# Optimization experiments

Hardware: AMD Instinct MI355X
Metric: run time of the kernel (lower is better)

## Reference

```python
import jax, jax.numpy as jnp
import numpy as np

H, L, N1, N2, N3 = 256, 141, 9, 34, 98
B, S = 64, 512

def setup_inputs() -> dict:
    key = jax.random.key(0)
    cnt = [0]
    def nrm(shape, s=0.05):
        cnt[0] += 1
        return jax.random.normal(jax.random.fold_in(key, cnt[0]), shape, jnp.float32) * s
    d = {}
    d['inputs'] = jax.random.randint(jax.random.fold_in(key, 1000), (B, S), 0, 30522)
    d['text_hidden'] = nrm((B, S, 768), 1.0)
    d['label_encoding'] = nrm((L, H), 1.0)
    d['w12'] = (jax.random.uniform(jax.random.fold_in(key, 1001), (N1, N2)) < 0.3).astype(jnp.float32)
    d['w23'] = (jax.random.uniform(jax.random.fold_in(key, 1002), (N2, N3)) < 0.3).astype(jnp.float32)
    d['fre12'] = jax.random.uniform(jax.random.fold_in(key, 1003), (N1, N2), jnp.float32)
    d['fre23'] = jax.random.uniform(jax.random.fold_in(key, 1004), (N2, N3), jnp.float32)
    for name in ['wi1', 'wf1', 'wo1', 'wu1', 'wi2', 'wf2', 'wo2', 'wu2']:
        d[name + '_W'] = nrm((H, H)); d[name + '_b'] = nrm((H,))
    for name in ['ui1', 'uf1', 'uo1', 'uu1', 'ui2', 'uf2', 'uo2', 'uu2']:
        d[name + '_W'] = nrm((H, H))
    d['mix_W'] = nrm((3 * H, H)); d['mix_b'] = nrm((H,))
    d['tt_W'] = nrm((768, H)); d['tt_b'] = nrm((H,))
    d['A'] = nrm((L, L)); d['Wp'] = nrm((H, H))
    d['out_W'] = nrm((L * H, L)); d['out_b'] = nrm((L,))
    return d

def reference(inputs, text_hidden, label_encoding, w12, w23, fre12, fre23,
              wi1_W, wi1_b, wf1_W, wf1_b, wo1_W, wo1_b, wu1_W, wu1_b,
              wi2_W, wi2_b, wf2_W, wf2_b, wo2_W, wo2_b, wu2_W, wu2_b,
              ui1_W, uf1_W, uo1_W, uu1_W, ui2_W, uf2_W, uo2_W, uu2_W,
              mix_W, mix_b, tt_W, tt_b, A, Wp, out_W, out_b):
    sig, tanh = jax.nn.sigmoid, jnp.tanh
    v1 = label_encoding[:N1]          # [N1,H]
    v2 = label_encoding[N1:N1 + N2]   # [N2,H]
    v3 = label_encoding[N1 + N2:]     # [N3,H]
    w21, w32 = w12.T, w23.T
    # --- top-down tree-LSTM (suffix 1) ---
    i11 = sig(v1 @ wi1_W + wi1_b); o11 = sig(v1 @ wo1_W + wo1_b); u11 = tanh(v1 @ wu1_W + wu1_b)
    c11 = i11 * u11; h11 = o11 * tanh(c11)
    h21t = w21 @ h11
    i21 = sig(v2 @ wi1_W + wi1_b + h21t @ ui1_W)
    f21 = sig(v2 @ wf1_W + wf1_b + h21t @ uf1_W)
    o21 = sig(v2 @ wo1_W + wo1_b + h21t @ uo1_W)
    u21 = tanh(v2 @ wu1_W + wu1_b + h21t @ uu1_W)
    c21 = i21 * u21 + f21 * (w21 @ c11); h21 = o21 * tanh(c21)
    h31t = w32 @ h21
    i31 = sig(v3 @ wi1_W + wi1_b + h31t @ ui1_W)
    f31 = sig(v3 @ wf1_W + wf1_b + h31t @ uf1_W)
    o31 = sig(v3 @ wo1_W + wo1_b + h31t @ uo1_W)
    u31 = tanh(v3 @ wu1_W + wu1_b + h31t @ uu1_W)
    c31 = i31 * u31 + f31 * (w32 @ c21); h31 = o31 * tanh(c31)
    # --- bottom-up tree-LSTM (suffix 2) ---
    i32 = sig(v3 @ wi2_W + wi2_b); o32 = sig(v3 @ wo2_W + wo2_b); u32 = tanh(v3 @ wu2_W + wu2_b)
    c32 = i32 * u32; h32 = o32 * tanh(c32)
    h22t = fre23 @ h32
    i22 = sig(v2 @ wi2_W + wi2_b + h22t @ ui2_W)
    f22 = sig((w32 @ v2) @ wf2_W + wf2_b + h32 @ uf2_W)   # [N3,H]
    o22 = sig(v2 @ wo2_W + wo2_b + h22t @ uo2_W)
    u22 = tanh(v2 @ wu2_W + wu2_b + h22t @ uu2_W)
    c22 = i22 * u22 + w23 @ (f22 * c32); h22 = o22 * tanh(c22)
    h12t = fre12 @ h22
    i12 = sig(v1 @ wi2_W + wi2_b + h12t @ ui2_W)
    f12 = sig((w21 @ v1) @ wf2_W + wf2_b + h22 @ uf2_W)   # [N2,H]
    o12 = sig(v1 @ wo2_W + wo2_b + h12t @ uo2_W)
    u12 = tanh(v1 @ wu2_W + wu2_b + h12t @ uu2_W)
    c12 = i12 * u12 + w12 @ (f12 * c22); h12 = o12 * tanh(c12)
    h1 = jnp.concatenate([h11, h12], axis=1)
    h2 = jnp.concatenate([h21, h22], axis=1)
    h3 = jnp.concatenate([h31, h32], axis=1)
    le = jnp.concatenate([h1, h2, h3], axis=0)            # [L,2H]
    temp = jax.nn.relu(A @ label_encoding @ Wp)           # [L,H]
    le = jnp.concatenate([le, temp], axis=1) @ mix_W + mix_b  # [L,H]
    # --- masked cross-attention pooling over text ---
    text = tanh(text_hidden @ tt_W + tt_b)                # [B,S,H]
    att = jnp.einsum('lh,bsh->bls', le, text)             # [B,L,S]
    pad = jnp.where((inputs == 0) | (inputs == 101) | (inputs == 102), -jnp.inf, 0.0).astype(text.dtype)
    att = jax.nn.softmax(att + pad[:, None, :], axis=2)
    features = jnp.einsum('bls,bsh->blh', att, text).reshape(inputs.shape[0], -1)  # [B,L*H]
    return sig(features @ out_W + out_b)                  # [B,L]
```

## Files before the change

kernel.cpp:

```cpp
#include <hip/hip_runtime.h>
#include <math.h>

static constexpr int H = 256, L = 141, N1 = 9, N2 = 34, N3 = 98;
static constexpr int B = 64, S = 512;

typedef __attribute__((ext_vector_type(8))) _Float16 f16x8;
typedef __attribute__((ext_vector_type(4))) float f32x4;

__device__ inline unsigned short f2h(float x) {
    _Float16 h = (_Float16)x;
    return __builtin_bit_cast(unsigned short, h);
}
__device__ inline float sigf(float x) { return 1.f / (1.f + __expf(-x)); }

__device__ inline void gload_lds16(const void* g, void* l) {
    __builtin_amdgcn_global_load_lds(
        (const __attribute__((address_space(1))) void*)g,
        (__attribute__((address_space(3))) void*)l, 16, 0, 0);
}

__global__ __launch_bounds__(256) void prep(
    const float* __restrict__ ttW, unsigned short* __restrict__ Bt,
    const float* __restrict__ outW, unsigned short* __restrict__ outWh)
{
    __shared__ unsigned short Tl[32][257];
    __shared__ unsigned short T2[64 * 65];
    const int tid = threadIdx.x;
    if (blockIdx.x < 24) {
        const int t = blockIdx.x;
        #pragma unroll
        for (int p = 0; p < 32; p++) {
            int lin = p * 256 + tid;
            int r = lin >> 8, c = lin & 255;
            Tl[r][c] = f2h(ttW[(long)(t * 32 + r) * 256 + c]);
        }
        __syncthreads();
        unsigned short v[32];
        #pragma unroll
        for (int kin = 0; kin < 32; kin++) v[kin] = Tl[kin][tid];
        uint4* dst = (uint4*)(Bt + ((long)t * 256 + tid) * 32);
        #pragma unroll
        for (int q = 0; q < 4; q++) dst[q] = ((const uint4*)v)[q];
    } else {
        const int u = blockIdx.x - 24;
        const int r0 = (u % 564) * 64, c0 = (u / 564) * 64;
        const int R = 36096, C = 141;
        #pragma unroll
        for (int p = 0; p < 16; p++) {
            int lin = p * 256 + tid;
            int r = lin >> 6, c = lin & 63;
            int gc = c0 + c;
            float v = (gc < C) ? outW[(long)(r0 + r) * C + gc] : 0.f;
            T2[c * 65 + r] = f2h(v);
        }
        __syncthreads();
        #pragma unroll
        for (int p = 0; p < 16; p++) {
            int lin = p * 256 + tid;
            int c = lin >> 6, r = lin & 63;
            if (c0 + c < C)
                outWh[(long)(c0 + c) * R + r0 + r] = T2[c * 65 + r];
        }
    }
}

__global__ __launch_bounds__(512, 4) void text_gemm3(
    const float* __restrict__ Af,
    const unsigned short* __restrict__ Bt,
    const float* __restrict__ bias,
    unsigned short* __restrict__ outH,
    unsigned short* __restrict__ outHT)
{
    __shared__ unsigned short smem[28672];
    unsigned short* As = smem;
    unsigned short* Bs = smem + 4096;
    unsigned short* T  = smem;

    const int tid  = threadIdx.x;
    const int wave = tid >> 6, lane = tid & 63;
    const int quad = lane >> 4, l16 = lane & 15;
    const int m0 = blockIdx.x * 64;
    const int wm = (wave >> 2) * 32;
    const int wn = (wave & 3) * 64;

    const int arow = tid >> 3;
    const int ac16 = tid & 7;
    const float* aSrc = Af + (long)(m0 + arow) * 768 + ac16 * 4;
    const int ac8d = ac16 ^ ((arow & 3) << 1);
    const int aWoff = arow * 32 + ac8d * 4;

    const int bsc = (lane & 3) ^ ((lane >> 3) & 3);
    const long bSrcOff0 = (long)(wave * 32 + (lane >> 2)) * 32 + bsc * 8;
    const long bSrcOff1 = bSrcOff0 + 16 * 32;
    const int bDst0 = (wave * 32) * 32, bDst1 = (wave * 32 + 16) * 32;

    int aro[2], bro[4];
    #pragma unroll
    for (int i = 0; i < 2; i++) {
        int r = wm + i * 16 + l16;
        aro[i] = r * 32 + ((quad * 2) ^ ((r & 3) << 1)) * 4;
    }
    #pragma unroll
    for (int j = 0; j < 4; j++) {
        int n = wn + j * 16 + l16;
        bro[j] = n * 32 + ((quad ^ ((n >> 1) & 3)) << 3);
    }

    f32x4 acc[2][4] = {};
    float4 ar0, ar1;

    auto issueB = [&](int kt, int pb) {
        const unsigned short* src = Bt + (long)kt * 8192;
        unsigned short* d = Bs + pb * 8192;
        gload_lds16(src + bSrcOff0, d + bDst0);
        gload_lds16(src + bSrcOff1, d + bDst1);
    };
    auto writeA = [&](const float4& v, int pa) {
        unsigned int p0 = f2h(v.x) | ((unsigned int)f2h(v.y) << 16);
        unsigned int p1 = f2h(v.z) | ((unsigned int)f2h(v.w) << 16);
        *(uint2*)&As[pa * 2048 + aWoff] = make_uint2(p0, p1);
    };

    ar0 = *(const float4*)(aSrc + 0 * 32);
    issueB(0, 0);
    ar1 = *(const float4*)(aSrc + 1 * 32);
    issueB(1, 1);
    asm volatile("s_waitcnt vmcnt(5)" ::: "memory");
    writeA(ar0, 0);
    asm volatile("s_waitcnt vmcnt(3)" ::: "memory");
    asm volatile("s_waitcnt lgkmcnt(0)" ::: "memory");
    asm volatile("s_barrier" ::: "memory");

    auto body = [&](int t, float4& arIn, float4& arOut, int pa, int pr) {
        int kt2 = (t + 2 <= 23) ? t + 2 : 23;
        arOut = *(const float4*)(aSrc + kt2 * 32);
        f16x8 a[2], b[4];
        const unsigned short* ab = As + pa * 2048;
        const unsigned short* bb = Bs + pr * 8192;
        #pragma unroll
        for (int i = 0; i < 2; i++) a[i] = *(const f16x8*)&ab[aro[i]];
        #pragma unroll
        for (int j = 0; j < 4; j++) b[j] = *(const f16x8*)&bb[bro[j]];
        #pragma unroll
        for (int i = 0; i < 2; i++)
            #pragma unroll
            for (int j = 0; j < 4; j++)
                acc[i][j] = __builtin_amdgcn_mfma_f32_16x16x32_f16(
                    a[i], b[j], acc[i][j], 0, 0, 0);
        asm volatile("s_waitcnt vmcnt(3)" ::: "memory");
        writeA(arIn, pa ^ 1);
        int pw = pr + 2; if (pw >= 3) pw -= 3;
        issueB(kt2, pw);
        asm volatile("s_waitcnt vmcnt(3)" ::: "memory");
        asm volatile("s_waitcnt lgkmcnt(0)" ::: "memory");
        asm volatile("s_barrier" ::: "memory");
    };

    int pr = 0;
    #pragma unroll 1
    for (int t = 0; t < 24; t += 2) {
        body(t,     ar1, ar0, t & 1 ? 1 : 0, pr);
        int pr1 = pr + 1; if (pr1 >= 3) pr1 -= 3;
        body(t + 1, ar0, ar1, 1, pr1);
        pr = pr1 + 1; if (pr >= 3) pr -= 3;
    }
    asm volatile("s_waitcnt vmcnt(0)" ::: "memory");
    __syncthreads();

    float bv[4];
    #pragma unroll
    for (int j = 0; j < 4; j++) bv[j] = bias[wn + j * 16 + l16];

    #pragma unroll
    for (int i = 0; i < 2; i++) {
        #pragma unroll
        for (int j = 0; j < 4; j++) {
            const int mlb = wm + i * 16 + quad * 4;
            const int n   = wn + j * 16 + l16;
            unsigned short hv[4];
            #pragma unroll
            for (int r = 0; r < 4; r++) {
                float v = tanhf(acc[i][j][r] + bv[j]);
                hv[r] = f2h(v);
                outH[(long)(m0 + mlb + r) * 256 + n] = hv[r];
            }
            uint2 p;
            p.x = hv[0] | ((unsigned int)hv[1] << 16);
            p.y = hv[2] | ((unsigned int)hv[3] << 16);
            *(uint2*)&T[n * 72 + mlb] = p;
        }
    }
    __syncthreads();
    {
        const int bb2 = m0 >> 9, s0 = m0 & 511;
        const int n = tid >> 1, half = tid & 1;
        const uint4* src = (const uint4*)&T[n * 72 + half * 32];
        uint4* dst = (uint4*)&outHT[((long)bb2 * 256 + n) * 512 + s0 + half * 32];
        dst[0] = src[0]; dst[1] = src[1];
        dst[2] = src[2]; dst[3] = src[3];
    }
}

__global__ __launch_bounds__(256) void gates_pre(
    const float* __restrict__ le,
    const float* W0, const float* W1, const float* W2, const float* W3,
    const float* W4, const float* W5, const float* W6,
    const float* b0, const float* b1, const float* b2, const float* b3,
    const float* b4, const float* b5, const float* b6,
    const float* __restrict__ Amat, const float* __restrict__ w23,
    const float* __restrict__ w12, const float* __restrict__ Wp,
    const float* __restrict__ wf2_W,
    float* __restrict__ G, float* __restrict__ tmpP,
    float* __restrict__ wv2f, float* __restrict__ wv1f)
{
    __shared__ float smem[768];
    const int tid = threadIdx.x;
    const int nl = tid & 63, ks = tid >> 6;
    if (blockIdx.x < 28 * 141) {
        const int u = blockIdx.x;
        const int bx = u % 28, m = u / 28;
        const int j = bx >> 2, x = bx & 3, n = x * 64 + nl;
        float* ls = smem; float* red = smem + 256;
        ls[tid] = le[(long)m * 256 + tid];
        __syncthreads();
        const float *W, *bb;
        switch (j) {
            case 0: W = W0; bb = b0; break;  case 1: W = W1; bb = b1; break;
            case 2: W = W2; bb = b2; break;  case 3: W = W3; bb = b3; break;
            case 4: W = W4; bb = b4; break;  case 5: W = W5; bb = b5; break;
            default: W = W6; bb = b6;
        }
        float a0 = 0, a1 = 0, a2 = 0, a3 = 0;
        for (int k = ks; k + 12 < 256; k += 16) {
            long o = (long)k * 256 + n;
            a0 += ls[k] * W[o];        a1 += ls[k + 4] * W[o + 1024];
            a2 += ls[k + 8] * W[o + 2048]; a3 += ls[k + 12] * W[o + 3072];
        }
        red[tid] = a0 + a1 + a2 + a3;
        __syncthreads();
        if (ks == 0)
            G[((long)j * 141 + m) * 256 + n] =
                red[nl] + red[64 + nl] + red[128 + nl] + red[192 + nl] + bb[n];
    } else {
        const int u = blockIdx.x - 28 * 141;
        const int x = u % 4, y = u / 4, n = x * 64 + nl;
        int job, m, K1;
        if (y < 141)      { job = 0; m = y;       K1 = 141; }
        else if (y < 239) { job = 1; m = y - 141; K1 = 34; }
        else              { job = 2; m = y - 239; K1 = 9; }
        float* cs = smem; float* t = smem + 256; float* red = smem + 512;
        if (tid < K1)
            cs[tid] = (job == 0) ? Amat[(long)m * 141 + tid]
                    : (job == 1) ? w23[(long)tid * 98 + m]
                                 : w12[(long)tid * 34 + m];
        __syncthreads();
        const float* s1 = (job == 1) ? le + 9 * 256 : le;
        float acc = 0;
        #pragma unroll 4
        for (int k = 0; k < K1; k++) acc += cs[k] * s1[(long)k * 256 + tid];
        t[tid] = acc;
        __syncthreads();
        const float* W = (job == 0) ? Wp : wf2_W;
        float a0 = 0, a1 = 0, a2 = 0, a3 = 0;
        for (int k = ks; k + 12 < 256; k += 16) {
            long o = (long)k * 256 + n;
            a0 += t[k] * W[o];        a1 += t[k + 4] * W[o + 1024];
            a2 += t[k + 8] * W[o + 2048]; a3 += t[k + 12] * W[o + 3072];
        }
        red[tid] = a0 + a1 + a2 + a3;
        __syncthreads();
        if (ks == 0) {
            float tot = red[nl] + red[64 + nl] + red[128 + nl] + red[192 + nl];
            if (job == 0)      tmpP[(long)m * 256 + n] = fmaxf(tot, 0.f);
            else if (job == 1) wv2f[(long)m * 256 + n] = tot;
            else               wv1f[(long)m * 256 + n] = tot;
        }
    }
}

__global__ __launch_bounds__(256) void ew1(
    const float* __restrict__ G, float* __restrict__ h11, float* __restrict__ c11,
    float* __restrict__ h32, float* __restrict__ c32)
{
    int y = blockIdx.x, n = threadIdx.x;
    if (y < 9) {
        int m = y;
        float iv = sigf(G[(0L * 141 + m) * 256 + n]);
        float ov = sigf(G[(2L * 141 + m) * 256 + n]);
        float uv = tanhf(G[(3L * 141 + m) * 256 + n]);
        float cv = iv * uv;
        c11[m * 256 + n] = cv; h11[m * 256 + n] = ov * tanhf(cv);
    } else {
        int r = y - 9, grow = 43 + r;
        float iv = sigf(G[(4L * 141 + grow) * 256 + n]);
        float ov = sigf(G[(5L * 141 + grow) * 256 + n]);
        float uv = tanhf(G[(6L * 141 + grow) * 256 + n]);
        float cv = iv * uv;
        c32[r * 256 + n] = cv; h32[r * 256 + n] = ov * tanhf(cv);
    }
}

__global__ __launch_bounds__(256) void chain_mm(int phase,
    const float* __restrict__ w12, const float* __restrict__ w23,
    const float* __restrict__ fre23, const float* __restrict__ fre12,
    const float* __restrict__ h11, const float* __restrict__ c11,
    const float* __restrict__ h32,
    const float* __restrict__ h21, const float* __restrict__ c21,
    const float* __restrict__ h22,
    const float* __restrict__ wv2f, const float* __restrict__ wv1f,
// ... 153 lines not shown
    const float* __restrict__ tmpP, const float* __restrict__ mix_W,
    const float* __restrict__ mix_b, unsigned short* __restrict__ le_h)
{
    __shared__ float ls[768];
    __shared__ float red[256];
    const int x = blockIdx.x, l = blockIdx.y;
    const int tid = threadIdx.x, nl = tid & 63, ks = tid >> 6, n = x * 64 + nl;
    const float *pa, *pb; int r;
    if (l < 9)       { pa = h11; pb = h12; r = l; }
    else if (l < 43) { pa = h21; pb = h22; r = l - 9; }
    else             { pa = h31; pb = h32; r = l - 43; }
    for (int j = tid; j < 768; j += 256) {
        float v;
        if (j < 256)      v = pa[r * 256 + j];
        else if (j < 512) v = pb[r * 256 + (j - 256)];
        else              v = tmpP[l * 256 + (j - 512)];
        ls[j] = v;
    }
    __syncthreads();
    float a0 = 0, a1 = 0, a2 = 0, a3 = 0;
    for (int k = ks; k + 12 < 768; k += 16) {
        long o = (long)k * 256 + n;
        a0 += ls[k] * mix_W[o];        a1 += ls[k + 4] * mix_W[o + 1024];
        a2 += ls[k + 8] * mix_W[o + 2048]; a3 += ls[k + 12] * mix_W[o + 3072];
    }
    red[tid] = a0 + a1 + a2 + a3;
    __syncthreads();
    if (ks == 0) {
        float tot = red[nl] + red[64 + nl] + red[128 + nl] + red[192 + nl] + mix_b[n];
        le_h[(long)l * 256 + n] = f2h(tot);
    }
}

__global__ __launch_bounds__(512, 1) void att_logits2(
    const unsigned short* __restrict__ le_h,
    const unsigned short* __restrict__ text_h,
    const int* __restrict__ tokens,
    unsigned short* __restrict__ att_h)
{
    __shared__ unsigned short A_s[64 * 256];
    __shared__ unsigned short Bs[2][512 * 32];
    __shared__ float redm[8][32];
    __shared__ float reds[8][32];
    const int tid  = threadIdx.x;
    const int wave = tid >> 6, lane = tid & 63;
    const int quad = lane >> 4, l16 = lane & 15;
    const int m0 = blockIdx.x * 64;
    const int b  = blockIdx.y;
    const int wm = (wave >> 2) * 32;
    const int wn = (wave & 3) * 128;

    const int bsc = (lane & 3) ^ ((lane >> 3) & 3);
    const long bOffBase = (long)(b * 512 + wave * 64 + (lane >> 2)) * 256 + bsc * 8;
    const int bDstBase = (wave * 64) * 32;
    auto issueB = [&](int kt, int pb) {
        #pragma unroll
        for (int q = 0; q < 4; q++)
            gload_lds16(text_h + bOffBase + (long)q * 16 * 256 + kt * 32,
                        &Bs[pb][bDstBase + q * 16 * 32]);
    };

    int abase[2], axm[2], bro[8];
    #pragma unroll
    for (int i = 0; i < 2; i++) {
        int r = wm + i * 16 + l16;
        abase[i] = r * 256; axm[i] = r & 7;
    }
    #pragma unroll
    for (int j = 0; j < 8; j++) {
        int n = wn + j * 16 + l16;
        bro[j] = n * 32 + ((quad ^ ((n >> 1) & 3)) << 3);
    }

    #pragma unroll
    for (int p = 0; p < 4; p++) {
        int row = p * 16 + (tid >> 5);
        int c   = tid & 31;
        int grow = m0 + row; if (grow > L - 1) grow = L - 1;
        gload_lds16(le_h + (long)grow * 256 + ((c ^ (row & 7)) << 3),
                    A_s + p * 4096 + wave * 512);
    }
    issueB(0, 0);
    issueB(1, 1);
    asm volatile("s_waitcnt vmcnt(4)" ::: "memory");
    asm volatile("s_barrier" ::: "memory");

    f32x4 acc[2][8] = {};
    #pragma unroll 1
    for (int t = 0; t < 8; t++) {
        const int pb = t & 1;
        f16x8 a[2], bf[8];
        #pragma unroll
        for (int i = 0; i < 2; i++)
            a[i] = *(const f16x8*)&A_s[abase[i] + (((t * 4 + quad) ^ axm[i]) << 3)];
        const unsigned short* bb = &Bs[pb][0];
        #pragma unroll
        for (int j = 0; j < 8; j++) bf[j] = *(const f16x8*)&bb[bro[j]];
        #pragma unroll
        for (int i = 0; i < 2; i++)
            #pragma unroll
            for (int j = 0; j < 8; j++)
                acc[i][j] = __builtin_amdgcn_mfma_f32_16x16x32_f16(
                    a[i], bf[j], acc[i][j], 0, 0, 0);
        if (t < 7) {
            asm volatile("s_waitcnt lgkmcnt(0)" ::: "memory");
            asm volatile("s_barrier" ::: "memory");
            int kt2 = (t + 2 <= 7) ? t + 2 : 7;
            issueB(kt2, pb);
            asm volatile("s_waitcnt vmcnt(4)" ::: "memory");
            asm volatile("s_barrier" ::: "memory");
        }
    }
    asm volatile("s_waitcnt vmcnt(0)" ::: "memory");

    float mvv[8];
    #pragma unroll
    for (int j = 0; j < 8; j++) {
        int gs = wn + j * 16 + l16;
        int tok = tokens[(long)b * 512 + gs];
        mvv[j] = (tok == 0 || tok == 101 || tok == 102) ? 1e30f : 0.f;
    }
    #pragma unroll
    for (int i = 0; i < 2; i++)
        #pragma unroll
        for (int j = 0; j < 8; j++)
            #pragma unroll
            for (int r = 0; r < 4; r++) acc[i][j][r] -= mvv[j];

// ... 27 lines not shown
    for (int i = 0; i < 2; i++)
        #pragma unroll
        for (int j = 0; j < 8; j++)
            #pragma unroll
            for (int r = 0; r < 4; r++) {
                float e = __expf(acc[i][j][r] - M[i][r]);
                acc[i][j][r] = e;
                psum[i][r] += e;
            }
    #pragma unroll
    for (int i = 0; i < 2; i++)
        #pragma unroll
        for (int r = 0; r < 4; r++) {
            float v = psum[i][r];
            #pragma unroll
            for (int d = 1; d <= 8; d <<= 1) v += __shfl_xor(v, d);
            if (l16 == 0) reds[wave][i * 16 + quad * 4 + r] = v;
        }
    __syncthreads();
    #pragma unroll
    for (int i = 0; i < 2; i++)
        #pragma unroll
        for (int r = 0; r < 4; r++) {
            int rl = i * 16 + quad * 4 + r;
            float s = reds[wgrp][rl] + reds[wgrp + 1][rl]
                    + reds[wgrp + 2][rl] + reds[wgrp + 3][rl];
            M[i][r] = 1.f / s;
        }

    #pragma unroll
    for (int i = 0; i < 2; i++)
        #pragma unroll
        for (int r = 0; r < 4; r++) {
            int gm = m0 + wm + i * 16 + quad * 4 + r;
            if (gm < L) {
                unsigned short* orow = att_h + ((long)b * L + gm) * 512;
                #pragma unroll
                for (int j = 0; j < 8; j++)
                    orow[wn + j * 16 + l16] = f2h(acc[i][j][r] * M[i][r]);
            }
        }
}

__global__ __launch_bounds__(512, 4) void att_pv(
    const unsigned short* __restrict__ att_h,
    const unsigned short* __restrict__ text_hT,
    unsigned short* __restrict__ feat_h)
{
    __shared__ unsigned short As[2 * 64 * 64];
    __shared__ unsigned short Bs[3][256 * 32];
    const int tid  = threadIdx.x;
    const int wave = tid >> 6, lane = tid & 63;
    const int quad = lane >> 4, l16 = lane & 15;
    const int m0 = blockIdx.x * 64;
    const int b  = blockIdx.y;
    const int wm = (wave >> 2) * 32;
    const int wn = (wave & 3) * 64;

    int arow = m0 + wave * 8 + (lane >> 3); if (arow > L - 1) arow = L - 1;
    const int asc = (lane & 7) ^ (lane >> 3);
    const unsigned short* aSrc = att_h + ((long)b * L + arow) * 512 + asc * 8;
    const int aDst = wave * 512;
    auto issueA = [&](int ka, int pa) {
        gload_lds16(aSrc + ka * 64, &As[pa * 4096 + aDst]);
    };

    const int bsc = (lane & 3) ^ ((lane >> 3) & 3);
    const long bOff0 = ((long)b * 256 + wave * 32 + (lane >> 2)) * 512 + bsc * 8;
    const long bOff1 = bOff0 + 16 * 512;
    const int bDst0 = (wave * 32) * 32, bDst1 = bDst0 + 16 * 32;
    auto issueB = [&](int kt, int pb) {
        gload_lds16(text_hT + bOff0 + kt * 32, &Bs[pb][bDst0]);
        gload_lds16(text_hT + bOff1 + kt * 32, &Bs[pb][bDst1]);
    };

    int aro[2], axm[2], bro[4];
    #pragma unroll
    for (int i = 0; i < 2; i++) {
        int r = wm + i * 16 + l16;
        aro[i] = r * 64; axm[i] = r & 7;
    }
    #pragma unroll
    for (int j = 0; j < 4; j++) {
        int n = wn + j * 16 + l16;
        bro[j] = n * 32 + ((quad ^ ((n >> 1) & 3)) << 3);
    }

    issueA(0, 0);
    issueB(0, 0);
    issueB(1, 1);
    asm volatile("s_waitcnt vmcnt(2)" ::: "memory");
    asm volatile("s_barrier" ::: "memory");

    f32x4 acc[2][4] = {};
    #pragma unroll 1
    for (int t = 0; t < 16; t++) {
        const int pa = (t >> 1) & 1, pr = t % 3, sub = t & 1;
        f16x8 a[2], bfr[4];
        const unsigned short* ab = &As[pa * 4096];
        #pragma unroll
        for (int i = 0; i < 2; i++)
            a[i] = *(const f16x8*)&ab[aro[i] + (((sub * 4 + quad) ^ axm[i]) << 3)];
        const unsigned short* bb = &Bs[pr][0];
        #pragma unroll
        for (int j = 0; j < 4; j++) bfr[j] = *(const f16x8*)&bb[bro[j]];
        #pragma unroll
        for (int i = 0; i < 2; i++)
            #pragma unroll
            for (int j = 0; j < 4; j++)
                acc[i][j] = __builtin_amdgcn_mfma_f32_16x16x32_f16(
                    a[i], bfr[j], acc[i][j], 0, 0, 0);
        if (t < 15) {
            if (sub == 0) {
                int ka = (t >> 1) + 1; if (ka > 7) ka = 7;
                issueA(ka, pa ^ 1);
            }
            int kb = t + 2; if (kb > 15) kb = 15;
            issueB(kb, (t + 2) % 3);
            if (sub == 0) {
                asm volatile("s_waitcnt vmcnt(3)" ::: "memory");
            } else {
                asm volatile("s_waitcnt vmcnt(2)" ::: "memory");
            }
            asm volatile("s_barrier" ::: "memory");
        }
    }
    asm volatile("s_waitcnt vmcnt(0)" ::: "memory");

    #pragma unroll
    for (int i = 0; i < 2; i++)
        #pragma unroll
        for (int j = 0; j < 4; j++)
            #pragma unroll
            for (int r = 0; r < 4; r++) {
                int gm = m0 + wm + i * 16 + quad * 4 + r;
                if (gm < L) {
                    int h = wn + j * 16 + l16;
                    feat_h[(long)b * (L * H) + (long)gm * 256 + h] =
                        f2h(acc[i][j][r]);
                }
            }
}

template<int EPI, bool CONVA, int IM>
__global__ __launch_bounds__(256) void gemm_mfma(
    const void* __restrict__ Aptr, int lda, long strA,
    const unsigned short* __restrict__ Bp, int ldb, long strB,
    float* __restrict__ C, int ldc, long strC,
    int M, int N, int K,
    const float* __restrict__ bias,
    const int* __restrict__ tokens,
    unsigned short* __restrict__ outH,
    unsigned short* __restrict__ outHT,
    int kChunk)
{
    __shared__ unsigned short A_s[32 * IM * 32];
    __shared__ unsigned short B_s[128 * 32];
    const int tid  = threadIdx.x;
    const int wave = tid >> 6, lane = tid & 63;
    const int quad = lane >> 4, l16 = lane & 15;
    const int bz = blockIdx.z;
    const int m0 = blockIdx.y * (32 * IM), n0 = blockIdx.x * 128;
    const int wm = (wave & 1) * (16 * IM), wn = (wave >> 1) * 64;

    long aBase, bBase;
    int kBeg, kEnd;
    if (EPI == 4) { aBase = 0; bBase = 0; kBeg = bz * kChunk; kEnd = kBeg + kChunk; }
    else { aBase = (long)bz * strA; bBase = (long)bz * strB; kBeg = 0; kEnd = K; }

    f32x4 acc[IM][4] = {};

    for (int k0 = kBeg; k0 < kEnd; k0 += 32) {
// ... 104 lines not shown
    const float* uo1_W = (const float*)d_in[25], *uu1_W = (const float*)d_in[26];
    const float* ui2_W = (const float*)d_in[27], *uf2_W = (const float*)d_in[28];
    const float* uo2_W = (const float*)d_in[29], *uu2_W = (const float*)d_in[30];
    const float* mix_W = (const float*)d_in[31], *mix_b = (const float*)d_in[32];
    const float* tt_W  = (const float*)d_in[33], *tt_b  = (const float*)d_in[34];
    const float* Amat  = (const float*)d_in[35], *Wp    = (const float*)d_in[36];
    const float* out_W = (const float*)d_in[37], *out_b = (const float*)d_in[38];
    float* out = (float*)d_out;

    float* ws = (float*)d_ws;
    float* att     = ws; ws += (long)B * L * S;
    unsigned short* text_h  = (unsigned short*)ws; ws += (long)B * S * H / 2;
    unsigned short* text_hT = (unsigned short*)ws; ws += (long)B * S * H / 2;
    unsigned short* att_h   = (unsigned short*)ws; ws += (long)B * L * S / 2;
    unsigned short* tt_Wt   = (unsigned short*)ws; ws += 768 * H / 2;
    unsigned short* le_h    = (unsigned short*)ws; ws += L * H / 2 + 4;
    unsigned short* out_Wh  = (unsigned short*)ws; ws += (long)L * 36096 / 2;
    unsigned short* feat_h  = (unsigned short*)ws; ws += (long)B * L * H / 2;
    float* outacc = ws; ws += (long)B * L * 141;
    float* G    = ws; ws += 7 * 141 * 256;
    float* tmpP = ws; ws += L * H;
    float* wv2f = ws; ws += N3 * H;
    float* wv1f = ws; ws += N2 * H;
    float* h11  = ws; ws += N1 * H;  float* c11  = ws; ws += N1 * H;
    float* h21  = ws; ws += N2 * H;  float* c21  = ws; ws += N2 * H;
    float* h21t = ws; ws += N2 * H;  float* c21p = ws; ws += N2 * H;
    float* h31  = ws; ws += N3 * H;  float* h31t = ws; ws += N3 * H;
    float* c31p = ws; ws += N3 * H;
    float* h32  = ws; ws += N3 * H;  float* c32  = ws; ws += N3 * H;
    float* h22  = ws; ws += N2 * H;  float* c22  = ws; ws += N2 * H;
    float* h22t = ws; ws += N2 * H;  float* fcb  = ws; ws += N3 * H;
    float* h12  = ws; ws += N1 * H;  float* h12t = ws; ws += N1 * H;
    float* fc2b = ws; ws += N2 * H;
    (void)att;

    prep<<<24 + 564 * 3, 256, 0, stream>>>(tt_W, tt_Wt, out_W, out_Wh);
    text_gemm3<<<512, 512, 0, stream>>>(
        text_hidden, tt_Wt, tt_b, text_h, text_hT);
    gates_pre<<<28 * 141 + 4 * 273, 256, 0, stream>>>(label_enc,
        wi1_W, wf1_W, wo1_W, wu1_W, wi2_W, wo2_W, wu2_W,
        wi1_b, wf1_b, wo1_b, wu1_b, wi2_b, wo2_b, wu2_b,
        Amat, w23, w12, Wp, wf2_W, G, tmpP, wv2f, wv1f);
    ew1<<<107, 256, 0, stream>>>(G, h11, c11, h32, c32);
    chain_mm<<<dim3(4, 200), 256, 0, stream>>>(0, w12, w23, fre23, fre12,
        h11, c11, h32, h21, c21, h22, wv2f, wv1f, wf2_b, uf2_W, c32, c22,
        h21t, c21p, h22t, fcb, h31t, c31p, h12t, fc2b);
    lstm_fused<<<dim3(4, 68), 256, 0, stream>>>(0, G,
        h21t, c21p, h22t, fcb, h31t, c31p, h12t, fc2b, w23, w12,
        ui1_W, uf1_W, uo1_W, uu1_W, ui2_W, uo2_W, uu2_W,
        h21, c21, h22, c22, h31, h12);
    chain_mm<<<dim3(4, 239), 256, 0, stream>>>(1, w12, w23, fre23, fre12,
        h11, c11, h32, h21, c21, h22, wv2f, wv1f, wf2_b, uf2_W, c32, c22,
        h21t, c21p, h22t, fcb, h31t, c31p, h12t, fc2b);
    lstm_fused<<<dim3(4, 107), 256, 0, stream>>>(1, G,
        h21t, c21p, h22t, fcb, h31t, c31p, h12t, fc2b, w23, w12,
        ui1_W, uf1_W, uo1_W, uu1_W, ui2_W, uo2_W, uu2_W,
        h21, c21, h22, c22, h31, h12);
    mix_mm<<<dim3(4, 141), 256, 0, stream>>>(h11, h12, h21, h22, h31, h32,
        tmpP, mix_W, mix_b, le_h);
    att_logits2<<<dim3(3, 64), 512, 0, stream>>>(
        le_h, text_h, inputs, att_h);
    att_pv<<<dim3(3, 64), 512, 0, stream>>>(att_h, text_hT, feat_h);
    gemm_mfma<4, false, 2><<<dim3(2, 1, 141), 256, 0, stream>>>(
        feat_h, L * H, 0, out_Wh, L * H, 0, outacc, L, (long)B * L,
        B, L, L * H, nullptr, nullptr, nullptr, nullptr, 256);
    out_final<<<(B * L + 255) / 256, 256, 0, stream>>>(outacc, out_b, out, B * L, 141);
}
```

Baseline: 439.3 us.

## Enlarge text GEMM tile to 128 rows with 1024-thread blocks

The text projection GEMM now uses 1024-thread blocks covering 128 rows each, so the B-operand tile loaded into LDS is shared by twice as many rows and each thread issues one B load per stage instead of two. Wait counts, A buffer sizes and the transposed-output epilogue are reworked, with the epilogue run in two halves through the shared staging buffer. The trade-off is only 256 blocks at one block per CU, which reduces occupancy and adds barriers in the epilogue.

New measurement: 443.1 us. About the same (+0.8%).

```diff
diff --git a/kernel.cpp b/kernel.cpp
--- a/kernel.cpp
+++ b/kernel.cpp
@@ -64,22 +64,22 @@
     }
 }
 
-__global__ __launch_bounds__(512, 4) void text_gemm3(
+__global__ __launch_bounds__(1024, 1) void text_gemm4(
     const float* __restrict__ Af,
     const unsigned short* __restrict__ Bt,
     const float* __restrict__ bias,
     unsigned short* __restrict__ outH,
     unsigned short* __restrict__ outHT)
 {
-    __shared__ unsigned short smem[28672];
+    __shared__ unsigned short smem[32768];
     unsigned short* As = smem;
-    unsigned short* Bs = smem + 4096;
+    unsigned short* Bs = smem + 8192;
     unsigned short* T  = smem;
 
     const int tid  = threadIdx.x;
     const int wave = tid >> 6, lane = tid & 63;
     const int quad = lane >> 4, l16 = lane & 15;
-    const int m0 = blockIdx.x * 64;
+    const int m0 = blockIdx.x * 128;
     const int wm = (wave >> 2) * 32;
     const int wn = (wave & 3) * 64;
 
@@ -90,9 +90,8 @@
     const int aWoff = arow * 32 + ac8d * 4;
 
     const int bsc = (lane & 3) ^ ((lane >> 3) & 3);
-    const long bSrcOff0 = (long)(wave * 32 + (lane >> 2)) * 32 + bsc * 8;
-    const long bSrcOff1 = bSrcOff0 + 16 * 32;
-    const int bDst0 = (wave * 32) * 32, bDst1 = (wave * 32 + 16) * 32;
+    const long bSrcOff = (long)(wave * 16 + (lane >> 2)) * 32 + bsc * 8;
+    const int bDst = (wave * 16) * 32;
 
     int aro[2], bro[4];
     #pragma unroll
@@ -110,24 +109,21 @@
     float4 ar0, ar1;
 
     auto issueB = [&](int kt, int pb) {
-        const unsigned short* src = Bt + (long)kt * 8192;
-        unsigned short* d = Bs + pb * 8192;
-        gload_lds16(src + bSrcOff0, d + bDst0);
-        gload_lds16(src + bSrcOff1, d + bDst1);
+        gload_lds16(Bt + (long)kt * 8192 + bSrcOff, Bs + pb * 8192 + bDst);
     };
     auto writeA = [&](const float4& v, int pa) {
         unsigned int p0 = f2h(v.x) | ((unsigned int)f2h(v.y) << 16);
         unsigned int p1 = f2h(v.z) | ((unsigned int)f2h(v.w) << 16);
-        *(uint2*)&As[pa * 2048 + aWoff] = make_uint2(p0, p1);
+        *(uint2*)&As[pa * 4096 + aWoff] = make_uint2(p0, p1);
     };
 
     ar0 = *(const float4*)(aSrc + 0 * 32);
     issueB(0, 0);
     ar1 = *(const float4*)(aSrc + 1 * 32);
     issueB(1, 1);
-    asm volatile("s_waitcnt vmcnt(5)" ::: "memory");
+    asm volatile("s_waitcnt vmcnt(3)" ::: "memory");
     writeA(ar0, 0);
-    asm volatile("s_waitcnt vmcnt(3)" ::: "memory");
+    asm volatile("s_waitcnt vmcnt(2)" ::: "memory");
     asm volatile("s_waitcnt lgkmcnt(0)" ::: "memory");
     asm volatile("s_barrier" ::: "memory");
 
@@ -135,7 +131,7 @@
         int kt2 = (t + 2 <= 23) ? t + 2 : 23;
         arOut = *(const float4*)(aSrc + kt2 * 32);
         f16x8 a[2], b[4];
-        const unsigned short* ab = As + pa * 2048;
+        const unsigned short* ab = As + pa * 4096;
         const unsigned short* bb = Bs + pr * 8192;
         #pragma unroll
         for (int i = 0; i < 2; i++) a[i] = *(const f16x8*)&ab[aro[i]];
@@ -147,11 +143,11 @@
             for (int j = 0; j < 4; j++)
                 acc[i][j] = __builtin_amdgcn_mfma_f32_16x16x32_f16(
                     a[i], b[j], acc[i][j], 0, 0, 0);
-        asm volatile("s_waitcnt vmcnt(3)" ::: "memory");
+        asm volatile("s_waitcnt vmcnt(2)" ::: "memory");
         writeA(arIn, pa ^ 1);
         int pw = pr + 2; if (pw >= 3) pw -= 3;
         issueB(kt2, pw);
-        asm volatile("s_waitcnt vmcnt(3)" ::: "memory");
+        asm volatile("s_waitcnt vmcnt(2)" ::: "memory");
         asm volatile("s_waitcnt lgkmcnt(0)" ::: "memory");
         asm volatile("s_barrier" ::: "memory");
     };
@@ -159,7 +155,7 @@
     int pr = 0;
     #pragma unroll 1
     for (int t = 0; t < 24; t += 2) {
-        body(t,     ar1, ar0, t & 1 ? 1 : 0, pr);
+        body(t,     ar1, ar0, 0, pr);
         int pr1 = pr + 1; if (pr1 >= 3) pr1 -= 3;
         body(t + 1, ar0, ar1, 1, pr1);
         pr = pr1 + 1; if (pr >= 3) pr -= 3;
@@ -170,34 +166,41 @@
     float bv[4];
     #pragma unroll
     for (int j = 0; j < 4; j++) bv[j] = bias[wn + j * 16 + l16];
-
-    #pragma unroll
-    for (int i = 0; i < 2; i++) {
-        #pragma unroll
-        for (int j = 0; j < 4; j++) {
-            const int mlb = wm + i * 16 + quad * 4;
-            const int n   = wn + j * 16 + l16;
-            unsigned short hv[4];
-            #pragma unroll
-            for (int r = 0; r < 4; r++) {
-                float v = tanhf(acc[i][j][r] + bv[j]);
-                hv[r] = f2h(v);
-                outH[(long)(m0 + mlb + r) * 256 + n] = hv[r];
+    const int bb2 = m0 >> 9, s0base = m0 & 511;
+    const int myhalf = wave >> 3;
+
+    #pragma unroll
+    for (int h = 0; h < 2; h++) {
+        __syncthreads();
+        if (myhalf == h) {
+            #pragma unroll
+            for (int i = 0; i < 2; i++) {
+                #pragma unroll
+                for (int j = 0; j < 4; j++) {
+                    const int mlb = wm + i * 16 + quad * 4;
+                    const int n   = wn + j * 16 + l16;
+                    unsigned short hv[4];
+                    #pragma unroll
+                    for (int r = 0; r < 4; r++) {
+                        float v = tanhf(acc[i][j][r] + bv[j]);
+                        hv[r] = f2h(v);
+                        outH[(long)(m0 + mlb + r) * 256 + n] = hv[r];
+                    }
+                    uint2 p;
+                    p.x = hv[0] | ((unsigned int)hv[1] << 16);
+                    p.y = hv[2] | ((unsigned int)hv[3] << 16);
+                    *(uint2*)&T[n * 72 + (mlb - h * 64)] = p;
+                }
             }
-            uint2 p;
-            p.x = hv[0] | ((unsigned int)hv[1] << 16);
-            p.y = hv[2] | ((unsigned int)hv[3] << 16);
-            *(uint2*)&T[n * 72 + mlb] = p;
-        }
-    }
-    __syncthreads();
-    {
-        const int bb2 = m0 >> 9, s0 = m0 & 511;
-        const int n = tid >> 1, half = tid & 1;
-        const uint4* src = (const uint4*)&T[n * 72 + half * 32];
-        uint4* dst = (uint4*)&outHT[((long)bb2 * 256 + n) * 512 + s0 + half * 32];
-        dst[0] = src[0]; dst[1] = src[1];
-        dst[2] = src[2]; dst[3] = src[3];
+        }
+        __syncthreads();
+        {
+            const int n = tid >> 2, q = tid & 3;
+            const uint4* src = (const uint4*)&T[n * 72 + q * 16];
+            uint4* dst = (uint4*)&outHT[((long)bb2 * 256 + n) * 512
+                                        + s0base + h * 64 + q * 16];
+            dst[0] = src[0]; dst[1] = src[1];
+        }
     }
 }
 
@@ -928,7 +931,7 @@
     (void)att;
 
     prep<<<24 + 564 * 3, 256, 0, stream>>>(tt_W, tt_Wt, out_W, out_Wh);
-    text_gemm3<<<512, 512, 0, stream>>>(
+    text_gemm4<<<256, 1024, 0, stream>>>(
         text_hidden, tt_Wt, tt_b, text_h, text_hT);
     gates_pre<<<28 * 141 + 4 * 273, 256, 0, stream>>>(label_enc,
         wi1_W, wf1_W, wo1_W, wu1_W, wi2_W, wo2_W, wu2_W,
```

## Fuse attention logits with PV matmul and merge prep with gate precompute

Applied to the files above, without the earlier changes.

Merges the attention-logit/softmax kernel with the P·V kernel so normalized probabilities stay in LDS (swizzled) instead of round-tripping through global memory. Also merges the weight-conversion prep kernel with the gate pre-activation kernel into one launch. A body() argument in text_gemm3 is simplified to a constant 0. This removes launches and the att_h global traffic, at the cost of larger LDS use in the fused attention kernel, which has launch bounds of 512 threads with min 1 block.

New measurement: 426.5 us. 1.03x faster.

```diff
diff --git a/kernel.cpp b/kernel.cpp
--- a/kernel.cpp
+++ b/kernel.cpp
@@ -19,30 +19,42 @@
         (__attribute__((address_space(3))) void*)l, 16, 0, 0);
 }
 
-__global__ __launch_bounds__(256) void prep(
+__global__ __launch_bounds__(256) void prep_gates(
     const float* __restrict__ ttW, unsigned short* __restrict__ Bt,
-    const float* __restrict__ outW, unsigned short* __restrict__ outWh)
+    const float* __restrict__ outW, unsigned short* __restrict__ outWh,
+    const float* __restrict__ le,
+    const float* W0, const float* W1, const float* W2, const float* W3,
+    const float* W4, const float* W5, const float* W6,
+    const float* b0, const float* b1, const float* b2, const float* b3,
+    const float* b4, const float* b5, const float* b6,
+    const float* __restrict__ Amat, const float* __restrict__ w23,
+    const float* __restrict__ w12, const float* __restrict__ Wp,
+    const float* __restrict__ wf2_W,
+    float* __restrict__ G, float* __restrict__ tmpP,
+    float* __restrict__ wv2f, float* __restrict__ wv1f)
 {
-    __shared__ unsigned short Tl[32][257];
-    __shared__ unsigned short T2[64 * 65];
+    __shared__ float sf[4112];
+    unsigned short* su = (unsigned short*)sf;
     const int tid = threadIdx.x;
-    if (blockIdx.x < 24) {
-        const int t = blockIdx.x;
+    const int bx = blockIdx.x;
+    const int nl = tid & 63, ks = tid >> 6;
+    if (bx < 24) {
+        const int t = bx;
         #pragma unroll
         for (int p = 0; p < 32; p++) {
             int lin = p * 256 + tid;
             int r = lin >> 8, c = lin & 255;
-            Tl[r][c] = f2h(ttW[(long)(t * 32 + r) * 256 + c]);
+            su[r * 257 + c] = f2h(ttW[(long)(t * 32 + r) * 256 + c]);
         }
         __syncthreads();
         unsigned short v[32];
         #pragma unroll
-        for (int kin = 0; kin < 32; kin++) v[kin] = Tl[kin][tid];
+        for (int kin = 0; kin < 32; kin++) v[kin] = su[kin * 257 + tid];
         uint4* dst = (uint4*)(Bt + ((long)t * 256 + tid) * 32);
         #pragma unroll
         for (int q = 0; q < 4; q++) dst[q] = ((const uint4*)v)[q];
-    } else {
-        const int u = blockIdx.x - 24;
+    } else if (bx < 24 + 1692) {
+        const int u = bx - 24;
         const int r0 = (u % 564) * 64, c0 = (u / 564) * 64;
         const int R = 36096, C = 141;
         #pragma unroll
@@ -51,7 +63,7 @@
             int r = lin >> 6, c = lin & 63;
             int gc = c0 + c;
             float v = (gc < C) ? outW[(long)(r0 + r) * C + gc] : 0.f;
-            T2[c * 65 + r] = f2h(v);
+            su[c * 65 + r] = f2h(v);
         }
         __syncthreads();
         #pragma unroll
@@ -59,7 +71,66 @@
             int lin = p * 256 + tid;
             int c = lin >> 6, r = lin & 63;
             if (c0 + c < C)
-                outWh[(long)(c0 + c) * R + r0 + r] = T2[c * 65 + r];
+                outWh[(long)(c0 + c) * R + r0 + r] = su[c * 65 + r];
+        }
+    } else if (bx < 24 + 1692 + 3948) {
+        const int u = bx - (24 + 1692);
+        const int bb = u % 28, m = u / 28;
+        const int j = bb >> 2, x = bb & 3, n = x * 64 + nl;
+        float* ls = sf; float* red = sf + 256;
+        ls[tid] = le[(long)m * 256 + tid];
+        __syncthreads();
+        const float *W, *bb2;
+        switch (j) {
+            case 0: W = W0; bb2 = b0; break;  case 1: W = W1; bb2 = b1; break;
+            case 2: W = W2; bb2 = b2; break;  case 3: W = W3; bb2 = b3; break;
+            case 4: W = W4; bb2 = b4; break;  case 5: W = W5; bb2 = b5; break;
+            default: W = W6; bb2 = b6;
+        }
+        float a0 = 0, a1 = 0, a2 = 0, a3 = 0;
+        for (int k = ks; k + 12 < 256; k += 16) {
+            long o = (long)k * 256 + n;
+            a0 += ls[k] * W[o];        a1 += ls[k + 4] * W[o + 1024];
+            a2 += ls[k + 8] * W[o + 2048]; a3 += ls[k + 12] * W[o + 3072];
+        }
+        red[tid] = a0 + a1 + a2 + a3;
+        __syncthreads();
+        if (ks == 0)
+            G[((long)j * 141 + m) * 256 + n] =
+                red[nl] + red[64 + nl] + red[128 + nl] + red[192 + nl] + bb2[n];
+    } else {
+        const int u = bx - (24 + 1692 + 3948);
+        const int x = u % 4, y = u / 4, n = x * 64 + nl;
+        int job, m, K1;
+        if (y < 141)      { job = 0; m = y;       K1 = 141; }
+        else if (y < 239) { job = 1; m = y - 141; K1 = 34; }
+        else              { job = 2; m = y - 239; K1 = 9; }
+        float* cs = sf; float* t = sf + 256; float* red = sf + 512;
+        if (tid < K1)
+            cs[tid] = (job == 0) ? Amat[(long)m * 141 + tid]
+                    : (job == 1) ? w23[(long)tid * 98 + m]
+                                 : w12[(long)tid * 34 + m];
+        __syncthreads();
+        const float* s1 = (job == 1) ? le + 9 * 256 : le;
+        float acc = 0;
+        #pragma unroll 4
+        for (int k = 0; k < K1; k++) acc += cs[k] * s1[(long)k * 256 + tid];
+        t[tid] = acc;
+        __syncthreads();
+        const float* W = (job == 0) ? Wp : wf2_W;
+        float a0 = 0, a1 = 0, a2 = 0, a3 = 0;
+        for (int k = ks; k + 12 < 256; k += 16) {
+            long o = (long)k * 256 + n;
+            a0 += t[k] * W[o];        a1 += t[k + 4] * W[o + 1024];
+            a2 += t[k + 8] * W[o + 2048]; a3 += t[k + 12] * W[o + 3072];
+        }
+        red[tid] = a0 + a1 + a2 + a3;
+        __syncthreads();
+        if (ks == 0) {
+            float tot = red[nl] + red[64 + nl] + red[128 + nl] + red[192 + nl];
+            if (job == 0)      tmpP[(long)m * 256 + n] = fmaxf(tot, 0.f);
+            else if (job == 1) wv2f[(long)m * 256 + n] = tot;
+            else               wv1f[(long)m * 256 + n] = tot;
         }
     }
 }
@@ -159,7 +230,7 @@
     int pr = 0;
     #pragma unroll 1
     for (int t = 0; t < 24; t += 2) {
-        body(t,     ar1, ar0, t & 1 ? 1 : 0, pr);
+        body(t,     ar1, ar0, 0, pr);
         int pr1 = pr + 1; if (pr1 >= 3) pr1 -= 3;
         body(t + 1, ar0, ar1, 1, pr1);
         pr = pr1 + 1; if (pr >= 3) pr -= 3;
@@ -198,83 +269,6 @@
         uint4* dst = (uint4*)&outHT[((long)bb2 * 256 + n) * 512 + s0 + half * 32];
         dst[0] = src[0]; dst[1] = src[1];
         dst[2] = src[2]; dst[3] = src[3];
-    }
-}
-
-__global__ __launch_bounds__(256) void gates_pre(
-    const float* __restrict__ le,
-    const float* W0, const float* W1, const float* W2, const float* W3,
-    const float* W4, const float* W5, const float* W6,
-    const float* b0, const float* b1, const float* b2, const float* b3,
-    const float* b4, const float* b5, const float* b6,
-    const float* __restrict__ Amat, const float* __restrict__ w23,
-    const float* __restrict__ w12, const float* __restrict__ Wp,
-    const float* __restrict__ wf2_W,
-    float* __restrict__ G, float* __restrict__ tmpP,
-    float* __restrict__ wv2f, float* __restrict__ wv1f)
-{
-    __shared__ float smem[768];
-    const int tid = threadIdx.x;
-    const int nl = tid & 63, ks = tid >> 6;
-    if (blockIdx.x < 28 * 141) {
-        const int u = blockIdx.x;
-        const int bx = u % 28, m = u / 28;
-        const int j = bx >> 2, x = bx & 3, n = x * 64 + nl;
-        float* ls = smem; float* red = smem + 256;
-        ls[tid] = le[(long)m * 256 + tid];
-        __syncthreads();
-        const float *W, *bb;
-        switch (j) {
-            case 0: W = W0; bb = b0; break;  case 1: W = W1; bb = b1; break;
-            case 2: W = W2; bb = b2; break;  case 3: W = W3; bb = b3; break;
-            case 4: W = W4; bb = b4; break;  case 5: W = W5; bb = b5; break;
-            default: W = W6; bb = b6;
-        }
-        float a0 = 0, a1 = 0, a2 = 0, a3 = 0;
-        for (int k = ks; k + 12 < 256; k += 16) {
-            long o = (long)k * 256 + n;
-            a0 += ls[k] * W[o];        a1 += ls[k + 4] * W[o + 1024];
-            a2 += ls[k + 8] * W[o + 2048]; a3 += ls[k + 12] * W[o + 3072];
-        }
-        red[tid] = a0 + a1 + a2 + a3;
-        __syncthreads();
-        if (ks == 0)
-            G[((long)j * 141 + m) * 256 + n] =
-                red[nl] + red[64 + nl] + red[128 + nl] + red[192 + nl] + bb[n];
-    } else {
-        const int u = blockIdx.x - 28 * 141;
-        const int x = u % 4, y = u / 4, n = x * 64 + nl;
-        int job, m, K1;
-        if (y < 141)      { job = 0; m = y;       K1 = 141; }
-        else if (y < 239) { job = 1; m = y - 141; K1 = 34; }
-        else              { job = 2; m = y - 239; K1 = 9; }
-        float* cs = smem; float* t = smem + 256; float* red = smem + 512;
-        if (tid < K1)
-            cs[tid] = (job == 0) ? Amat[(long)m * 141 + tid]
-                    : (job == 1) ? w23[(long)tid * 98 + m]
-                                 : w12[(long)tid * 34 + m];
-        __syncthreads();
-        const float* s1 = (job == 1) ? le + 9 * 256 : le;
-        float acc = 0;
-        #pragma unroll 4
-        for (int k = 0; k < K1; k++) acc += cs[k] * s1[(long)k * 256 + tid];
-        t[tid] = acc;
-        __syncthreads();
-        const float* W = (job == 0) ? Wp : wf2_W;
-        float a0 = 0, a1 = 0, a2 = 0, a3 = 0;
-        for (int k = ks; k + 12 < 256; k += 16) {
-            long o = (long)k * 256 + n;
-            a0 += t[k] * W[o];        a1 += t[k + 4] * W[o + 1024];
-            a2 += t[k + 8] * W[o + 2048]; a3 += t[k + 12] * W[o + 3072];
-        }
-        red[tid] = a0 + a1 + a2 + a3;
-        __syncthreads();
-        if (ks == 0) {
-            float tot = red[nl] + red[64 + nl] + red[128 + nl] + red[192 + nl];
-            if (job == 0)      tmpP[(long)m * 256 + n] = fmaxf(tot, 0.f);
-            else if (job == 1) wv2f[(long)m * 256 + n] = tot;
-            else               wv1f[(long)m * 256 + n] = tot;
-        }
     }
 }
 
@@ -494,16 +488,21 @@
     }
 }
 
-__global__ __launch_bounds__(512, 1) void att_logits2(
+__global__ __launch_bounds__(512, 1) void att_fused(
     const unsigned short* __restrict__ le_h,
     const unsigned short* __restrict__ text_h,
+    const unsigned short* __restrict__ text_hT,
     const int* __restrict__ tokens,
-    unsigned short* __restrict__ att_h)
+    unsigned short* __restrict__ feat_h)
 {
-    __shared__ unsigned short A_s[64 * 256];
-    __shared__ unsigned short Bs[2][512 * 32];
+    __shared__ unsigned short smem[57344];
     __shared__ float redm[8][32];
     __shared__ float reds[8][32];
+    unsigned short* A_s = smem;
+    unsigned short* BsL = smem + 16384;
+    unsigned short* P   = smem;
+    unsigned short* Vb  = smem + 32768;
+
     const int tid  = threadIdx.x;
     const int wave = tid >> 6, lane = tid & 63;
     const int quad = lane >> 4, l16 = lane & 15;
@@ -519,7 +518,7 @@
         #pragma unroll
         for (int q = 0; q < 4; q++)
             gload_lds16(text_h + bOffBase + (long)q * 16 * 256 + kt * 32,
-                        &Bs[pb][bDstBase + q * 16 * 32]);
+                        &BsL[pb * 16384 + bDstBase + q * 16 * 32]);
     };
 
     int abase[2], axm[2], bro[8];
@@ -555,7 +554,7 @@
         #pragma unroll
         for (int i = 0; i < 2; i++)
             a[i] = *(const f16x8*)&A_s[abase[i] + (((t * 4 + quad) ^ axm[i]) << 3)];
-        const unsigned short* bb = &Bs[pb][0];
+        const unsigned short* bb = &BsL[pb * 16384];
         #pragma unroll
         for (int j = 0; j < 8; j++) bf[j] = *(const f16x8*)&bb[bro[j]];
         #pragma unroll
@@ -649,96 +648,64 @@
     for (int i = 0; i < 2; i++)
         #pragma unroll
         for (int r = 0; r < 4; r++) {
-            int gm = m0 + wm + i * 16 + quad * 4 + r;
-            if (gm < L) {
-                unsigned short* orow = att_h + ((long)b * L + gm) * 512;
-                #pragma unroll
-                for (int j = 0; j < 8; j++)
-                    orow[wn + j * 16 + l16] = f2h(acc[i][j][r] * M[i][r]);
+            int ml = wm + i * 16 + quad * 4 + r;
+            int gm = m0 + ml;
+            #pragma unroll
+            for (int j = 0; j < 8; j++) {
+                int col = wn + j * 16 + l16;
+                float pv = (gm < L) ? acc[i][j][r] * M[i][r] : 0.f;
+                int c = col >> 3, w = col & 7;
+                P[ml * 512 + ((c ^ (ml & 7)) << 3) + w] = f2h(pv);
             }
         }
-}
-
-__global__ __launch_bounds__(512, 4) void att_pv(
-    const unsigned short* __restrict__ att_h,
-    const unsigned short* __restrict__ text_hT,
-    unsigned short* __restrict__ feat_h)
-{
-    __shared__ unsigned short As[2 * 64 * 64];
-    __shared__ unsigned short Bs[3][256 * 32];
-    const int tid  = threadIdx.x;
-    const int wave = tid >> 6, lane = tid & 63;
-    const int quad = lane >> 4, l16 = lane & 15;
-    const int m0 = blockIdx.x * 64;
-    const int b  = blockIdx.y;
-    const int wm = (wave >> 2) * 32;
-    const int wn = (wave & 3) * 64;
-
-    int arow = m0 + wave * 8 + (lane >> 3); if (arow > L - 1) arow = L - 1;
-    const int asc = (lane & 7) ^ (lane >> 3);
-    const unsigned short* aSrc = att_h + ((long)b * L + arow) * 512 + asc * 8;
-    const int aDst = wave * 512;
-    auto issueA = [&](int ka, int pa) {
-        gload_lds16(aSrc + ka * 64, &As[pa * 4096 + aDst]);
+
+    const int wnp = (wave & 3) * 64;
+    const long vOff0 = ((long)b * 256 + wave * 32 + (lane >> 2)) * 512 + bsc * 8;
+    const long vOff1 = vOff0 + 16 * 512;
+    const int vDst0 = (wave * 32) * 32, vDst1 = vDst0 + 16 * 32;
+    auto issueV = [&](int kt, int pb) {
+        gload_lds16(text_hT + vOff0 + kt * 32, Vb + pb * 8192 + vDst0);
+        gload_lds16(text_hT + vOff1 + kt * 32, Vb + pb * 8192 + vDst1);
     };
-
-    const int bsc = (lane & 3) ^ ((lane >> 3) & 3);
-    const long bOff0 = ((long)b * 256 + wave * 32 + (lane >> 2)) * 512 + bsc * 8;
-    const long bOff1 = bOff0 + 16 * 512;
-    const int bDst0 = (wave * 32) * 32, bDst1 = bDst0 + 16 * 32;
-    auto issueB = [&](int kt, int pb) {
-        gload_lds16(text_hT + bOff0 + kt * 32, &Bs[pb][bDst0]);
-        gload_lds16(text_hT + bOff1 + kt * 32, &Bs[pb][bDst1]);
-    };
-
-    int aro[2], axm[2], bro[4];
+    int paro[2], pxm[2], vro[4];
     #pragma unroll
     for (int i = 0; i < 2; i++) {
         int r = wm + i * 16 + l16;
-        aro[i] = r * 64; axm[i] = r & 7;
+        paro[i] = r * 512; pxm[i] = r & 7;
     }
     #pragma unroll
     for (int j = 0; j < 4; j++) {
-        int n = wn + j * 16 + l16;
-        bro[j] = n * 32 + ((quad ^ ((n >> 1) & 3)) << 3);
-    }
-
-    issueA(0, 0);
-    issueB(0, 0);
-    issueB(1, 1);
+        int n = wnp + j * 16 + l16;
+        vro[j] = n * 32 + ((quad ^ ((n >> 1) & 3)) << 3);
+    }
+
+    issueV(0, 0);
+    issueV(1, 1);
+    asm volatile("s_waitcnt lgkmcnt(0)" ::: "memory");
     asm volatile("s_waitcnt vmcnt(2)" ::: "memory");
     asm volatile("s_barrier" ::: "memory");
 
-    f32x4 acc[2][4] = {};
+    f32x4 accp[2][4] = {};
     #pragma unroll 1
     for (int t = 0; t < 16; t++) {
-        const int pa = (t >> 1) & 1, pr = t % 3, sub = t & 1;
-        f16x8 a[2], bfr[4];
-        const unsigned short* ab = &As[pa * 4096];
+        const int pr = t % 3;
+        f16x8 a2[2], vf[4];
         #pragma unroll
         for (int i = 0; i < 2; i++)
-            a[i] = *(const f16x8*)&ab[aro[i] + (((sub * 4 + quad) ^ axm[i]) << 3)];
-        const unsigned short* bb = &Bs[pr][0];
-        #pragma unroll
-        for (int j = 0; j < 4; j++) bfr[j] = *(const f16x8*)&bb[bro[j]];
+            a2[i] = *(const f16x8*)&P[paro[i] + (((t * 4 + quad) ^ pxm[i]) << 3)];
+        const unsigned short* vb = Vb + pr * 8192;
+        #pragma unroll
+        for (int j = 0; j < 4; j++) vf[j] = *(const f16x8*)&vb[vro[j]];
         #pragma unroll
         for (int i = 0; i < 2; i++)
             #pragma unroll
             for (int j = 0; j < 4; j++)
-                acc[i][j] = __builtin_amdgcn_mfma_f32_16x16x32_f16(
-                    a[i], bfr[j], acc[i][j], 0, 0, 0);
+                accp[i][j] = __builtin_amdgcn_mfma_f32_16x16x32_f16(
+                    a2[i], vf[j], accp[i][j], 0, 0, 0);
         if (t < 15) {
-            if (sub == 0) {
-                int ka = (t >> 1) + 1; if (ka > 7) ka = 7;
-                issueA(ka, pa ^ 1);
-            }
             int kb = t + 2; if (kb > 15) kb = 15;
-            issueB(kb, (t + 2) % 3);
-            if (sub == 0) {
-                asm volatile("s_waitcnt vmcnt(3)" ::: "memory");
-            } else {
-                asm volatile("s_waitcnt vmcnt(2)" ::: "memory");
-            }
+            issueV(kb, (t + 2) % 3);
+            asm volatile("s_waitcnt vmcnt(2)" ::: "memory");
             asm volatile("s_barrier" ::: "memory");
         }
     }
@@ -752,9 +719,9 @@
             for (int r = 0; r < 4; r++) {
                 int gm = m0 + wm + i * 16 + quad * 4 + r;
                 if (gm < L) {
-                    int h = wn + j * 16 + l16;
+                    int h = wnp + j * 16 + l16;
                     feat_h[(long)b * (L * H) + (long)gm * 256 + h] =
-                        f2h(acc[i][j][r]);
+                        f2h(accp[i][j][r]);
                 }
             }
 }
@@ -925,15 +892,15 @@
     float* h22t = ws; ws += N2 * H;  float* fcb  = ws; ws += N3 * H;
     float* h12  = ws; ws += N1 * H;  float* h12t = ws; ws += N1 * H;
     float* fc2b = ws; ws += N2 * H;
-    (void)att;
-
-    prep<<<24 + 564 * 3, 256, 0, stream>>>(tt_W, tt_Wt, out_W, out_Wh);
-    text_gemm3<<<512, 512, 0, stream>>>(
-        text_hidden, tt_Wt, tt_b, text_h, text_hT);
-    gates_pre<<<28 * 141 + 4 * 273, 256, 0, stream>>>(label_enc,
+    (void)att; (void)att_h;
+
+    prep_gates<<<24 + 1692 + 3948 + 1092, 256, 0, stream>>>(
+        tt_W, tt_Wt, out_W, out_Wh, label_enc,
         wi1_W, wf1_W, wo1_W, wu1_W, wi2_W, wo2_W, wu2_W,
         wi1_b, wf1_b, wo1_b, wu1_b, wi2_b, wo2_b, wu2_b,
         Amat, w23, w12, Wp, wf2_W, G, tmpP, wv2f, wv1f);
+    text_gemm3<<<512, 512, 0, stream>>>(
+        text_hidden, tt_Wt, tt_b, text_h, text_hT);
     ew1<<<107, 256, 0, stream>>>(G, h11, c11, h32, c32);
     chain_mm<<<dim3(4, 200), 256, 0, stream>>>(0, w12, w23, fre23, fre12,
         h11, c11, h32, h21, c21, h22, wv2f, wv1f, wf2_b, uf2_W, c32, c22,
@@ -951,9 +918,8 @@
         h21, c21, h22, c22, h31, h12);
     mix_mm<<<dim3(4, 141), 256, 0, stream>>>(h11, h12, h21, h22, h31, h32,
         tmpP, mix_W, mix_b, le_h);
-    att_logits2<<<dim3(3, 64), 512, 0, stream>>>(
-        le_h, text_h, inputs, att_h);
-    att_pv<<<dim3(3, 64), 512, 0, stream>>>(att_h, text_hT, feat_h);
+    att_fused<<<dim3(3, 64), 512, 0, stream>>>(
+        le_h, text_h, text_hT, inputs, feat_h);
     gemm_mfma<4, false, 2><<<dim3(2, 1, 141), 256, 0, stream>>>(
         feat_h, L * H, 0, out_Wh, L * H, 0, outacc, L, (long)B * L,
         B, L, L * H, nullptr, nullptr, nullptr, nullptr, 256);
```
